# Optimization experiments

Measured on AMD Instinct MI355X. Metric: run time of the kernel, lower is better.

The kernel has to match this reference:

```python
import jax, jax.numpy as jnp
import numpy as np

TOP_K = 2
NUM_EXPERTS = 8


def setup_inputs() -> dict:
    key = jax.random.key(0)
    ks = jax.random.split(key, 9)
    B, S, N, H = 1, 8, 1024, 512
    E, I_moe, I_sh = NUM_EXPERTS, 2048 // TOP_K, 2048
    s = 0.02
    return {
        "hidden_states": jax.random.normal(ks[0], (B, S, N, H), dtype=jnp.float32),
        "gate_w": jax.random.normal(ks[1], (E, H), dtype=jnp.float32) * s,
        "expert_w1": jax.random.normal(ks[2], (E, I_moe, H), dtype=jnp.float32) * s,
        "expert_w2": jax.random.normal(ks[3], (E, H, I_moe), dtype=jnp.float32) * s,
        "expert_w3": jax.random.normal(ks[4], (E, I_moe, H), dtype=jnp.float32) * s,
        "shared_w1": jax.random.normal(ks[5], (I_sh, H), dtype=jnp.float32) * s,
        "shared_w2": jax.random.normal(ks[6], (H, I_sh), dtype=jnp.float32) * s,
        "shared_w3": jax.random.normal(ks[7], (I_sh, H), dtype=jnp.float32) * s,
        "shared_gate_w": jax.random.normal(ks[8], (1, H), dtype=jnp.float32) * s,
    }


def reference(hidden_states, gate_w, expert_w1, expert_w2, expert_w3,
              shared_w1, shared_w2, shared_w3, shared_gate_w):
    B, S, N, H = hidden_states.shape
    x = hidden_states.reshape(-1, H)                       # [T, H], T = B*S*N

    # Router: softmax in fp32, then top-k (norm_topk_prob=False).
    router_logits = x @ gate_w.T                           # [T, E]
    probs = jax.nn.softmax(router_logits.astype(jnp.float32), axis=-1)
    top_w, top_i = jax.lax.top_k(probs, TOP_K)             # [T, k]
    # Combine weight per (token, expert): zero for unselected experts.
    combine = jnp.sum(top_w[..., None] * jax.nn.one_hot(top_i, NUM_EXPERTS, dtype=probs.dtype), axis=1)
    combine = combine.astype(x.dtype)                      # [T, E]

    # Routed experts (SwiGLU FFN per expert), evaluated densely and masked
    # by the sparse combine weights (same math as gather/scatter dispatch).
    h1 = jnp.einsum('th,eih->tei', x, expert_w1)           # [T, E, I_moe]
    h3 = jnp.einsum('th,eih->tei', x, expert_w3)
    h = jax.nn.silu(h1) * h3
    expert_out = jnp.einsum('tei,ehi->teh', h, expert_w2)  # [T, E, H]
    moe_out = jnp.einsum('te,teh->th', combine, expert_out)

    # Shared expert with sigmoid gate.
    sh = (jax.nn.silu(x @ shared_w1.T) * (x @ shared_w3.T)) @ shared_w2.T
    sgate = jax.nn.sigmoid(x @ shared_gate_w.T)            # [T, 1]
    out = moe_out + sgate * sh

    return out.reshape(B, S, N, H), router_logits
```

## Files before the change

### kernel.cpp

```cpp
#include <hip/hip_runtime.h>
#include <hip/hip_bf16.h>
#include <stdint.h>
#include <math.h>

typedef __bf16 bf16;
typedef bf16 bf16x8 __attribute__((ext_vector_type(8)));
typedef bf16 bf16x4 __attribute__((ext_vector_type(4)));
typedef float f32x4 __attribute__((ext_vector_type(4)));
typedef unsigned int u32;

#define TOKENS 8192
#define HD 512
#define NE 8
#define IM 1024
#define ISH 2048
#define CAP 2560

__device__ __forceinline__ void gld16(const void* g, void* l) {
  __builtin_amdgcn_global_load_lds(
      (const __attribute__((address_space(1))) u32*)g,
      (__attribute__((address_space(3))) u32*)l, 16, 0, 0);
}

#define F4_X  (TOKENS * HD / 4)
#define F4_E  (NE * IM * HD / 4)
#define F4_S  (ISH * HD / 4)
#define F4_B1 (F4_X)
#define F4_B2 (F4_B1 + F4_E)
#define F4_B3 (F4_B2 + F4_E)
#define F4_B4 (F4_B3 + F4_E)
#define F4_B5 (F4_B4 + F4_S)
#define F4_B6 (F4_B5 + F4_S)
#define F4_TOT (F4_B6 + F4_S)

__global__ void cvt_all(const float* __restrict__ x, const float* __restrict__ e1,
                        const float* __restrict__ e3, const float* __restrict__ e2,
                        const float* __restrict__ s1, const float* __restrict__ s3,
                        const float* __restrict__ s2, bf16* __restrict__ dst) {
  int i = blockIdx.x * 256 + threadIdx.x;
  if (i >= F4_TOT) return;
  const float* s; int off;
  if (i < F4_B1)      { s = x;  off = i; }
  else if (i < F4_B2) { s = e1; off = i - F4_B1; }
  else if (i < F4_B3) { s = e3; off = i - F4_B2; }
  else if (i < F4_B4) { s = e2; off = i - F4_B3; }
  else if (i < F4_B5) { s = s1; off = i - F4_B4; }
  else if (i < F4_B6) { s = s3; off = i - F4_B5; }
  else                { s = s2; off = i - F4_B6; }
  const float4 v = ((const float4*)s)[off];
  bf16x4 o;
  o.x = (bf16)v.x; o.y = (bf16)v.y; o.z = (bf16)v.z; o.w = (bf16)v.w;
  ((bf16x4*)dst)[i] = o;
}

__launch_bounds__(256)
__global__ void router_k(const float* __restrict__ x, const float* __restrict__ gw,
                         const float* __restrict__ sgw, float* __restrict__ logits,
                         float* __restrict__ sgate, int* __restrict__ topi,
                         float* __restrict__ topw, int* __restrict__ counts,
                         float* __restrict__ outz) {
  {
    float4 z = {0.f, 0.f, 0.f, 0.f};
    float4* op = (float4*)(outz + (size_t)blockIdx.x * 2048);
    op[threadIdx.x] = z;
    op[threadIdx.x + 256] = z;
  }
  if (blockIdx.x == 0 && threadIdx.x < NE) counts[threadIdx.x] = 0;
  __shared__ float gws[9][512];
  for (int i = threadIdx.x; i < 9 * 512; i += 256) {
    int r = i >> 9, c = i & 511;
    gws[r][c] = (r < 8) ? gw[i] : sgw[c];
  }
  __syncthreads();
  int wave = threadIdx.x >> 6, lane = threadIdx.x & 63;
  int t = blockIdx.x * 4 + wave;
  const float* xp = x + (size_t)t * HD;
  float xv[8];
#pragma unroll
  for (int j = 0; j < 8; j++) xv[j] = xp[lane + 64 * j];
  float acc[9];
#pragma unroll
  for (int e = 0; e < 9; e++) {
    float a = 0.f;
#pragma unroll
    for (int j = 0; j < 8; j++) a = fmaf(xv[j], gws[e][lane + 64 * j], a);
    acc[e] = a;
  }
#pragma unroll
  for (int off = 32; off > 0; off >>= 1) {
#pragma unroll
    for (int e = 0; e < 9; e++) acc[e] += __shfl_down(acc[e], off);
  }
  if (lane == 0) {
    float mx = acc[0];
#pragma unroll
    for (int e = 1; e < 8; e++) mx = fmaxf(mx, acc[e]);
    float p[8], sum = 0.f;
#pragma unroll
    for (int e = 0; e < 8; e++) { p[e] = expf(acc[e] - mx); sum += p[e]; }
    float inv = 1.f / sum;
    int i0 = 0; float b0 = p[0];
#pragma unroll
    for (int e = 1; e < 8; e++) if (p[e] > b0) { b0 = p[e]; i0 = e; }
    int i1 = -1; float b1 = -1.f;
#pragma unroll
    for (int e = 0; e < 8; e++) if (e != i0 && p[e] > b1) { b1 = p[e]; i1 = e; }
#pragma unroll
    for (int e = 0; e < 8; e++) logits[(size_t)t * 8 + e] = acc[e];
    topi[2 * t] = i0; topi[2 * t + 1] = i1;
    topw[2 * t] = b0 * inv; topw[2 * t + 1] = b1 * inv;
    sgate[t] = 1.f / (1.f + expf(-acc[8]));
  }
}

__launch_bounds__(256)
__global__ void dispatch_k(const int* __restrict__ topi, const float* __restrict__ topw,
                           int* __restrict__ counts, int* __restrict__ tok,
                           float* __restrict__ wl) {
  __shared__ int lcnt[NE];
  __shared__ int lbase[NE];
  int tid = threadIdx.x;
  if (tid < NE) lcnt[tid] = 0;
  __syncthreads();
  int t = blockIdx.x * 256 + tid;
  int e0 = topi[2 * t], e1 = topi[2 * t + 1];
  float w0 = topw[2 * t], w1 = topw[2 * t + 1];
  int r0 = atomicAdd(&lcnt[e0], 1);
  int r1 = atomicAdd(&lcnt[e1], 1);
  __syncthreads();
  if (tid < NE) lbase[tid] = atomicAdd(&counts[tid], lcnt[tid]);
  __syncthreads();
  int p0 = lbase[e0] + r0;
  int p1 = lbase[e1] + r1;
  if (p0 < CAP) { tok[e0 * CAP + p0] = t; wl[e0 * CAP + p0] = w0; }
  if (p1 < CAP) { tok[e1 * CAP + p1] = t; wl[e1 * CAP + p1] = w1; }
}

__launch_bounds__(256, 2)
__global__ void gemm1_k(const bf16* __restrict__ X, const int* __restrict__ tokl,
                        const int* __restrict__ counts,
                        const bf16* __restrict__ e1w, const bf16* __restrict__ e3w,
                        const bf16* __restrict__ s1w, const bf16* __restrict__ s3w,
                        bf16* __restrict__ hmoe, bf16* __restrict__ hsh) {
  const bf16 *W1, *W3;
  bf16* Hout;
  const int* tl = nullptr;
  int cnt = 0, m0, n0, N;
  bool gather;
  int y = blockIdx.y;
  if (y < 160) {
    int e = y / 20, mt = y % 20;
    cnt = min(counts[e], CAP);
    if (mt * 128 >= cnt) return;
    gather = true;
    tl = tokl + e * CAP;
    W1 = e1w + (size_t)e * IM * HD;
    W3 = e3w + (size_t)e * IM * HD;
    Hout = hmoe + (size_t)e * CAP * IM;
    N = IM; m0 = mt * 128; n0 = blockIdx.x * 64;
  } else {
    int s = y - 160;
    gather = false;
    W1 = s1w; W3 = s3w; Hout = hsh; N = ISH;
    m0 = (s >> 1) * 128;
    n0 = ((s & 1) * 16 + blockIdx.x) * 64;
  }

  __shared__ __align__(16) bf16 As[2][128 * 32];
  __shared__ __align__(16) bf16 B1s[2][64 * 32];
  __shared__ __align__(16) bf16 B3s[2][64 * 32];

  int tid = threadIdx.x;
  int sr = tid >> 2;
  int colb = (tid & 3) * 16;
  int ar0, ar1;
  if (gather) {
    ar0 = tl[min(m0 + sr, cnt - 1)];
    ar1 = tl[min(m0 + 64 + sr, cnt - 1)];
  } else { ar0 = m0 + sr; ar1 = m0 + 64 + sr; }
  const char* apa = (const char*)(X + (size_t)ar0 * HD) + colb;
  const char* apb = (const char*)(X + (size_t)ar1 * HD) + colb;
  const char* bp1 = (const char*)(W1 + (size_t)(n0 + sr) * HD) + colb;
  const char* bp3 = (const char*)(W3 + (size_t)(n0 + sr) * HD) + colb;
  char* lA0a = (char*)&As[0][0] + tid * 16;
  char* lA0b = (char*)&As[1][0] + tid * 16;
  char* lA1a = (char*)&As[0][0] + 4096 + tid * 16;
  char* lA1b = (char*)&As[1][0] + 4096 + tid * 16;
  char* lB1a = (char*)&B1s[0][0] + tid * 16;
  char* lB1b = (char*)&B1s[1][0] + tid * 16;
  char* lB3a = (char*)&B3s[0][0] + tid * 16;
  char* lB3b = (char*)&B3s[1][0] + tid * 16;

  int wid = tid >> 6, lane = tid & 63;
  int wm = (wid >> 1) * 64, wn = (wid & 1) * 32;
  int lrow = lane & 15, lq = lane >> 4;

  f32x4 acc1[4][2] = {};
  f32x4 acc3[4][2] = {};

  for (int kb = 0; kb < 1024; kb += 128) {
    __syncthreads();
    gld16(apa + kb, lA0a);      gld16(apa + kb + 64, lA0b);
    gld16(apb + kb, lA1a);      gld16(apb + kb + 64, lA1b);
    gld16(bp1 + kb, lB1a);      gld16(bp1 + kb + 64, lB1b);
    gld16(bp3 + kb, lB3a);      gld16(bp3 + kb + 64, lB3b);
    __syncthreads();
#pragma unroll
    for (int ks = 0; ks < 2; ks++) {
      bf16x8 a[4], b1[2], b3[2];
#pragma unroll
      for (int i = 0; i < 4; i++)
        a[i] = *(const bf16x8*)&As[ks][(wm + i * 16 + lrow) * 32 + lq * 8];
#pragma unroll
      for (int j = 0; j < 2; j++) {
        b1[j] = *(const bf16x8*)&B1s[ks][(wn + j * 16 + lrow) * 32 + lq * 8];
        b3[j] = *(const bf16x8*)&B3s[ks][(wn + j * 16 + lrow) * 32 + lq * 8];
      }
#pragma unroll
      for (int i = 0; i < 4; i++)
#pragma unroll
        for (int j = 0; j < 2; j++) {
          acc1[i][j] = __builtin_amdgcn_mfma_f32_16x16x32_bf16(a[i], b1[j], acc1[i][j], 0, 0, 0);
          acc3[i][j] = __builtin_amdgcn_mfma_f32_16x16x32_bf16(a[i], b3[j], acc3[i][j], 0, 0, 0);
        }
    }
  }

#pragma unroll
  for (int i = 0; i < 4; i++)
#pragma unroll
    for (int r = 0; r < 4; r++) {
      int row = m0 + wm + i * 16 + lq * 4 + r;
#pragma unroll
      for (int j = 0; j < 2; j++) {
        float v1 = acc1[i][j][r], v3 = acc3[i][j][r];
        float hv = v1 / (1.f + __expf(-v1)) * v3;
        Hout[(size_t)row * N + (n0 + wn + j * 16 + lrow)] = (bf16)hv;
      }
    }
}

__launch_bounds__(256, 2)
__global__ void gemm2_k(const bf16* __restrict__ hmoe, const bf16* __restrict__ hsh,
                        const bf16* __restrict__ e2w, const bf16* __restrict__ s2w,
                        const int* __restrict__ tokl, const float* __restrict__ wll,
                        const int* __restrict__ counts, const float* __restrict__ sgate,
                        float* __restrict__ out) {
  const bf16 *Hin, *W2;
  const int* tl = nullptr;
  const float* wlp = nullptr;
  int cnt = 0, m0, K;
  bool scatter;
  int y = blockIdx.y;
  if (y < 160) {
    int e = y / 20, mt = y % 20;
    cnt = min(counts[e], CAP);
    if (mt * 128 >= cnt) return;
    scatter = true;
    Hin = hmoe + (size_t)e * CAP * IM;
    W2 = e2w + (size_t)e * HD * IM;
    tl = tokl + e * CAP;
    wlp = wll + e * CAP;
    K = IM; m0 = mt * 128;
  } else {
    scatter = false;
    Hin = hsh; W2 = s2w; K = ISH; m0 = (y - 160) * 128;
  }
  int n0 = blockIdx.x * 128;

  __shared__ __align__(16) bf16 As[128 * 32];
  __shared__ __align__(16) bf16 Bs[128 * 32];

  int tid = threadIdx.x;
  int sr = tid >> 2;
  int colb = (tid & 3) * 16;
  const char* apa = (const char*)(Hin + (size_t)(m0 + sr) * K) + colb;
  const char* apb = (const char*)(Hin + (size_t)(m0 + 64 + sr) * K) + colb;
  const char* bpa = (const char*)(W2 + (size_t)(n0 + sr) * K) + colb;
  const char* bpb = (const char*)(W2 + (size_t)(n0 + 64 + sr) * K) + colb;
  char* lA0 = (char*)As + tid * 16;
  char* lA1 = (char*)As + 4096 + tid * 16;
  char* lB0 = (char*)Bs + tid * 16;
  char* lB1 = (char*)Bs + 4096 + tid * 16;

  int wid = tid >> 6, lane = tid & 63;
  int wm = (wid >> 1) * 64, wn = (wid & 1) * 64;
  int lrow = lane & 15, lq = lane >> 4;

  f32x4 acc[4][4] = {};

  for (int kb = 0; kb < K * 2; kb += 64) {
    __syncthreads();
    gld16(apa + kb, lA0);
    gld16(apb + kb, lA1);
    gld16(bpa + kb, lB0);
    gld16(bpb + kb, lB1);
    __syncthreads();
    bf16x8 a[4], b[4];
#pragma unroll
    for (int i = 0; i < 4; i++) {
      a[i] = *(const bf16x8*)&As[(wm + i * 16 + lrow) * 32 + lq * 8];
      b[i] = *(const bf16x8*)&Bs[(wn + i * 16 + lrow) * 32 + lq * 8];
    }
#pragma unroll
    for (int i = 0; i < 4; i++)
#pragma unroll
      for (int j = 0; j < 4; j++)
        acc[i][j] = __builtin_amdgcn_mfma_f32_16x16x32_bf16(a[i], b[j], acc[i][j], 0, 0, 0);
  }

#pragma unroll
  for (int i = 0; i < 4; i++)
#pragma unroll
    for (int r = 0; r < 4; r++) {
      int row = m0 + wm + i * 16 + lq * 4 + r;
      if (scatter) {
        if (row < cnt) {
          int t = tl[row];
          float w = wlp[row];
          float* op = out + (size_t)t * HD + n0;
#pragma unroll
          for (int j = 0; j < 4; j++)
            atomicAdd(op + wn + j * 16 + lrow, w * acc[i][j][r]);
        }
      } else {
        float g = sgate[row];
        float* op = out + (size_t)row * HD + n0;
#pragma unroll
        for (int j = 0; j < 4; j++)
          atomicAdd(op + wn + j * 16 + lrow, g * acc[i][j][r]);
      }
    }
}

extern "C" void kernel_launch(void* const* d_in, const int* in_sizes, int n_in,
                              void* d_out, int out_size, void* d_ws, size_t ws_size,
                              hipStream_t stream) {
  const float* x   = (const float*)d_in[0];
  const float* gw  = (const float*)d_in[1];
  const float* ew1 = (const float*)d_in[2];
  const float* ew2 = (const float*)d_in[3];
  const float* ew3 = (const float*)d_in[4];
  const float* sw1 = (const float*)d_in[5];
  const float* sw2 = (const float*)d_in[6];
  const float* sw3 = (const float*)d_in[7];
  const float* sgw = (const float*)d_in[8];
  float* out = (float*)d_out;
  float* logits = out + (size_t)TOKENS * HD;

  char* w = (char*)d_ws;
  bf16* xb  = (bf16*)w; w += (size_t)TOKENS * HD * 2;
  bf16* e1b = (bf16*)w; w += (size_t)NE * IM * HD * 2;
  bf16* e3b = (bf16*)w; w += (size_t)NE * IM * HD * 2;
  bf16* e2b = (bf16*)w; w += (size_t)NE * HD * IM * 2;
  bf16* s1b = (bf16*)w; w += (size_t)ISH * HD * 2;
  bf16* s3b = (bf16*)w; w += (size_t)ISH * HD * 2;
  bf16* s2b = (bf16*)w; w += (size_t)HD * ISH * 2;
  float* sgate = (float*)w; w += TOKENS * 4;
  int*   topi  = (int*)w;   w += TOKENS * 2 * 4;
  float* topw  = (float*)w; w += TOKENS * 2 * 4;
  int*   counts = (int*)w;  w += 256;
  int*   tok   = (int*)w;   w += NE * CAP * 4;
  float* wl    = (float*)w; w += NE * CAP * 4;
  bf16* hmoe = (bf16*)w; w += (size_t)NE * CAP * IM * 2;
  bf16* hsh  = (bf16*)w; w += (size_t)TOKENS * ISH * 2;

  hipLaunchKernelGGL(cvt_all, dim3((F4_TOT + 255) / 256), dim3(256), 0, stream,
                     x, ew1, ew3, ew2, sw1, sw3, sw2, xb);
  hipLaunchKernelGGL(router_k, dim3(TOKENS / 4), dim3(256), 0, stream,
                     x, gw, sgw, logits, sgate, topi, topw, counts, out);
  hipLaunchKernelGGL(dispatch_k, dim3(TOKENS / 256), dim3(256), 0, stream,
                     topi, topw, counts, tok, wl);
  hipLaunchKernelGGL(gemm1_k, dim3(16, 160 + 128), dim3(256), 0, stream,
                     xb, tok, counts, e1b, e3b, s1b, s3b, hmoe, hsh);
  hipLaunchKernelGGL(gemm2_k, dim3(4, 160 + 64), dim3(256), 0, stream,
                     hmoe, hsh, e2b, s2b, tok, wl, counts, sgate, out);
}
```

Baseline: 303.0 us.

## Replace atomic scatter-add in down-projection with slot buffers and a combine kernel

The down-projection GEMM used to scatter fp32 results into the output with atomicAdd, once per routed expert and once for the shared expert. It now writes routing-weighted results as bf16 into per-slot buffers and the shared result into its own buffer. A new combine kernel gathers each token's two expert slots plus the gated shared result and writes the output once, so the output zeroing and the atomics go away. The new buffers reuse the dead bf16 input and first-layer weight space, and the workspace layout is reordered so the second-layer weights stay live. The cost is an extra kernel launch and bf16 rounding of the partial results before summation, which may reduce accuracy.

```diff
diff --git a/kernel.cpp b/kernel.cpp
--- a/kernel.cpp
+++ b/kernel.cpp
@@ -28,14 +28,14 @@
 #define F4_B1 (F4_X)
 #define F4_B2 (F4_B1 + F4_E)
 #define F4_B3 (F4_B2 + F4_E)
-#define F4_B4 (F4_B3 + F4_E)
+#define F4_B4 (F4_B3 + F4_S)
 #define F4_B5 (F4_B4 + F4_S)
-#define F4_B6 (F4_B5 + F4_S)
+#define F4_B6 (F4_B5 + F4_E)
 #define F4_TOT (F4_B6 + F4_S)
 
 __global__ void cvt_all(const float* __restrict__ x, const float* __restrict__ e1,
-                        const float* __restrict__ e3, const float* __restrict__ e2,
-                        const float* __restrict__ s1, const float* __restrict__ s3,
+                        const float* __restrict__ e3, const float* __restrict__ s1,
+                        const float* __restrict__ s3, const float* __restrict__ e2,
                         const float* __restrict__ s2, bf16* __restrict__ dst) {
   int i = blockIdx.x * 256 + threadIdx.x;
   if (i >= F4_TOT) return;
@@ -43,9 +43,9 @@
   if (i < F4_B1)      { s = x;  off = i; }
   else if (i < F4_B2) { s = e1; off = i - F4_B1; }
   else if (i < F4_B3) { s = e3; off = i - F4_B2; }
-  else if (i < F4_B4) { s = e2; off = i - F4_B3; }
-  else if (i < F4_B5) { s = s1; off = i - F4_B4; }
-  else if (i < F4_B6) { s = s3; off = i - F4_B5; }
+  else if (i < F4_B4) { s = s1; off = i - F4_B3; }
+  else if (i < F4_B5) { s = s3; off = i - F4_B4; }
+  else if (i < F4_B6) { s = e2; off = i - F4_B5; }
   else                { s = s2; off = i - F4_B6; }
   const float4 v = ((const float4*)s)[off];
   bf16x4 o;
@@ -57,14 +57,7 @@
 __global__ void router_k(const float* __restrict__ x, const float* __restrict__ gw,
                          const float* __restrict__ sgw, float* __restrict__ logits,
                          float* __restrict__ sgate, int* __restrict__ topi,
-                         float* __restrict__ topw, int* __restrict__ counts,
-                         float* __restrict__ outz) {
-  {
-    float4 z = {0.f, 0.f, 0.f, 0.f};
-    float4* op = (float4*)(outz + (size_t)blockIdx.x * 2048);
-    op[threadIdx.x] = z;
-    op[threadIdx.x + 256] = z;
-  }
+                         float* __restrict__ topw, int* __restrict__ counts) {
   if (blockIdx.x == 0 && threadIdx.x < NE) counts[threadIdx.x] = 0;
   __shared__ float gws[9][512];
   for (int i = threadIdx.x; i < 9 * 512; i += 256) {
@@ -116,7 +109,7 @@
 __launch_bounds__(256)
 __global__ void dispatch_k(const int* __restrict__ topi, const float* __restrict__ topw,
                            int* __restrict__ counts, int* __restrict__ tok,
-                           float* __restrict__ wl) {
+                           float* __restrict__ wl, int* __restrict__ pos) {
   __shared__ int lcnt[NE];
   __shared__ int lbase[NE];
   int tid = threadIdx.x;
@@ -134,6 +127,8 @@
   int p1 = lbase[e1] + r1;
   if (p0 < CAP) { tok[e0 * CAP + p0] = t; wl[e0 * CAP + p0] = w0; }
   if (p1 < CAP) { tok[e1 * CAP + p1] = t; wl[e1 * CAP + p1] = w1; }
+  pos[2 * t]     = (p0 < CAP) ? e0 * CAP + p0 : -1;
+  pos[2 * t + 1] = (p1 < CAP) ? e1 * CAP + p1 : -1;
 }
 
 __launch_bounds__(256, 2)
@@ -243,28 +238,27 @@
 __launch_bounds__(256, 2)
 __global__ void gemm2_k(const bf16* __restrict__ hmoe, const bf16* __restrict__ hsh,
                         const bf16* __restrict__ e2w, const bf16* __restrict__ s2w,
-                        const int* __restrict__ tokl, const float* __restrict__ wll,
-                        const int* __restrict__ counts, const float* __restrict__ sgate,
-                        float* __restrict__ out) {
+                        const float* __restrict__ wll, const int* __restrict__ counts,
+                        bf16* __restrict__ yslot, bf16* __restrict__ ysh) {
   const bf16 *Hin, *W2;
-  const int* tl = nullptr;
   const float* wlp = nullptr;
+  bf16* Yout;
   int cnt = 0, m0, K;
-  bool scatter;
+  bool weighted;
   int y = blockIdx.y;
   if (y < 160) {
     int e = y / 20, mt = y % 20;
     cnt = min(counts[e], CAP);
     if (mt * 128 >= cnt) return;
-    scatter = true;
+    weighted = true;
     Hin = hmoe + (size_t)e * CAP * IM;
     W2 = e2w + (size_t)e * HD * IM;
-    tl = tokl + e * CAP;
     wlp = wll + e * CAP;
+    Yout = yslot + (size_t)e * CAP * HD;
     K = IM; m0 = mt * 128;
   } else {
-    scatter = false;
-    Hin = hsh; W2 = s2w; K = ISH; m0 = (y - 160) * 128;
+    weighted = false;
+    Hin = hsh; W2 = s2w; Yout = ysh; K = ISH; m0 = (y - 160) * 128;
   }
   int n0 = blockIdx.x * 128;
 
@@ -314,23 +308,42 @@
 #pragma unroll
     for (int r = 0; r < 4; r++) {
       int row = m0 + wm + i * 16 + lq * 4 + r;
-      if (scatter) {
-        if (row < cnt) {
-          int t = tl[row];
-          float w = wlp[row];
-          float* op = out + (size_t)t * HD + n0;
-#pragma unroll
-          for (int j = 0; j < 4; j++)
-            atomicAdd(op + wn + j * 16 + lrow, w * acc[i][j][r]);
-        }
-      } else {
-        float g = sgate[row];
-        float* op = out + (size_t)row * HD + n0;
-#pragma unroll
-        for (int j = 0; j < 4; j++)
-          atomicAdd(op + wn + j * 16 + lrow, g * acc[i][j][r]);
-      }
+      float w = weighted ? ((row < cnt) ? wlp[row] : 0.f) : 1.f;
+      bf16* op = Yout + (size_t)row * HD;
+#pragma unroll
+      for (int j = 0; j < 4; j++)
+        op[n0 + wn + j * 16 + lrow] = (bf16)(w * acc[i][j][r]);
     }
+}
+
+__launch_bounds__(256)
+__global__ void combine_k(const bf16* __restrict__ yslot, const bf16* __restrict__ ysh,
+                          const int* __restrict__ pos, const float* __restrict__ sgate,
+                          float* __restrict__ out) {
+  int wave = threadIdx.x >> 6, lane = threadIdx.x & 63;
+  int t = blockIdx.x * 4 + wave;
+  int p0 = pos[2 * t], p1 = pos[2 * t + 1];
+  float g = sgate[t];
+  int col = lane * 8;
+  float acc[8];
+  {
+    const bf16x8 s = *(const bf16x8*)(ysh + (size_t)t * HD + col);
+#pragma unroll
+    for (int i = 0; i < 8; i++) acc[i] = g * (float)s[i];
+  }
+  if (p0 >= 0) {
+    const bf16x8 v = *(const bf16x8*)(yslot + (size_t)p0 * HD + col);
+#pragma unroll
+    for (int i = 0; i < 8; i++) acc[i] += (float)v[i];
+  }
+  if (p1 >= 0) {
+    const bf16x8 v = *(const bf16x8*)(yslot + (size_t)p1 * HD + col);
+#pragma unroll
+    for (int i = 0; i < 8; i++) acc[i] += (float)v[i];
+  }
+  float* op = out + (size_t)t * HD + col;
+#pragma unroll
+  for (int i = 0; i < 8; i++) op[i] = acc[i];
 }
 
 extern "C" void kernel_launch(void* const* d_in, const int* in_sizes, int n_in,
@@ -352,9 +365,9 @@
   bf16* xb  = (bf16*)w; w += (size_t)TOKENS * HD * 2;
   bf16* e1b = (bf16*)w; w += (size_t)NE * IM * HD * 2;
   bf16* e3b = (bf16*)w; w += (size_t)NE * IM * HD * 2;
-  bf16* e2b = (bf16*)w; w += (size_t)NE * HD * IM * 2;
   bf16* s1b = (bf16*)w; w += (size_t)ISH * HD * 2;
   bf16* s3b = (bf16*)w; w += (size_t)ISH * HD * 2;
+  bf16* e2b = (bf16*)w; w += (size_t)NE * HD * IM * 2;
   bf16* s2b = (bf16*)w; w += (size_t)HD * ISH * 2;
   float* sgate = (float*)w; w += TOKENS * 4;
   int*   topi  = (int*)w;   w += TOKENS * 2 * 4;
@@ -362,17 +375,22 @@
   int*   counts = (int*)w;  w += 256;
   int*   tok   = (int*)w;   w += NE * CAP * 4;
   float* wl    = (float*)w; w += NE * CAP * 4;
+  int*   pos   = (int*)w;   w += TOKENS * 2 * 4;
   bf16* hmoe = (bf16*)w; w += (size_t)NE * CAP * IM * 2;
   bf16* hsh  = (bf16*)w; w += (size_t)TOKENS * ISH * 2;
+  bf16* yslot = xb;
+  bf16* ysh   = (bf16*)((char*)xb + (size_t)NE * CAP * HD * 2);
 
   hipLaunchKernelGGL(cvt_all, dim3((F4_TOT + 255) / 256), dim3(256), 0, stream,
-                     x, ew1, ew3, ew2, sw1, sw3, sw2, xb);
+                     x, ew1, ew3, sw1, sw3, ew2, sw2, xb);
   hipLaunchKernelGGL(router_k, dim3(TOKENS / 4), dim3(256), 0, stream,
-                     x, gw, sgw, logits, sgate, topi, topw, counts, out);
+                     x, gw, sgw, logits, sgate, topi, topw, counts);
   hipLaunchKernelGGL(dispatch_k, dim3(TOKENS / 256), dim3(256), 0, stream,
-                     topi, topw, counts, tok, wl);
+                     topi, topw, counts, tok, wl, pos);
   hipLaunchKernelGGL(gemm1_k, dim3(16, 160 + 128), dim3(256), 0, stream,
                      xb, tok, counts, e1b, e3b, s1b, s3b, hmoe, hsh);
   hipLaunchKernelGGL(gemm2_k, dim3(4, 160 + 64), dim3(256), 0, stream,
-                     hmoe, hsh, e2b, s2b, tok, wl, counts, sgate, out);
-}
+                     hmoe, hsh, e2b, s2b, wl, counts, yslot, ysh);
+  hipLaunchKernelGGL(combine_k, dim3(TOKENS / 4), dim3(256), 0, stream,
+                     yslot, ysh, pos, sgate, out);
+}
```

Measured after the change: 295.4 us. -2.5%, faster.
